# Performance work log

Hardware: AMD Instinct MI355X
Metric: run time of the kernel (lower is better)

The kernel has to match this reference:

```python
import jax, jax.numpy as jnp
import numpy as np

B, H, K, V = 64, 32, 128, 128


def setup_inputs() -> dict:
    key = jax.random.key(0)
    ks = jax.random.split(key, 7)
    q = jax.random.normal(ks[0], (B, 1, H, K), dtype=jnp.float32)
    k = jax.random.normal(ks[1], (B, 1, H, K), dtype=jnp.float32)
    v = jax.random.normal(ks[2], (B, 1, H, V), dtype=jnp.float32)
    # a = -kappa, b = kappa*a_gate in RWKV-7; plain gaussians suffice for a math reference
    a = jax.random.normal(ks[3], (B, 1, H, K), dtype=jnp.float32)
    b = jax.random.normal(ks[4], (B, 1, H, K), dtype=jnp.float32)
    # gk is a log-decay: negative so exp(gk) in (0, 1]
    gk = -jnp.abs(jax.random.normal(ks[5], (B, 1, H, K), dtype=jnp.float32)) * 0.1
    h0 = jax.random.normal(ks[6], (B, H, K, V), dtype=jnp.float32) * 0.1
    return {"q": q, "k": k, "v": v, "a": a, "b": b, "gk": gk, "h0": h0}


def reference(q, k, v, a, b, gk, h0):
    """RWKV-7 DPLR single-step (T=1) decode recurrence, per (batch, head):
      g     = exp(gk)                                # [K] decay
      s     = a^T H0                                 # [V]
      t     = (q*g)^T H0                             # [V]
      alpha = q . b ; beta = q . k                   # scalars
      o     = t + alpha*s + beta*v                   # [V]
      Ht    = diag(g) H0 + b s^T + k v^T             # [K,V]
    Mirrors dplr_decode_t1_kernel_streamK exactly (fp32 accumulation).
    """
    qf = q[:, 0].astype(jnp.float32)   # [B,H,K]
    kf = k[:, 0].astype(jnp.float32)
    af = a[:, 0].astype(jnp.float32)
    bf = b[:, 0].astype(jnp.float32)
    vf = v[:, 0].astype(jnp.float32)   # [B,H,V]
    g = jnp.exp(gk[:, 0].astype(jnp.float32))  # [B,H,K]
    hf = h0.astype(jnp.float32)        # [B,H,K,V]

    s = jnp.einsum('bhk,bhkv->bhv', af, hf)
    t = jnp.einsum('bhk,bhkv->bhv', qf * g, hf)
    alpha = jnp.sum(qf * bf, axis=-1, keepdims=True)  # [B,H,1]
    beta = jnp.sum(qf * kf, axis=-1, keepdims=True)   # [B,H,1]
    o = t + alpha * s + beta * vf                      # [B,H,V]

    ht = g[..., None] * hf + bf[..., None] * s[:, :, None, :] + kf[..., None] * vf[:, :, None, :]
    return o[:, None].astype(v.dtype), ht.astype(h0.dtype)
```

## Files before the change

kernel.cpp:

```cpp
#include <hip/hip_runtime.h>


#define KD 128
#define VD 128
#define BH_TOTAL 2048

__global__ __launch_bounds__(256, 4) void dplr_decode_t1_kernel(
    const float* __restrict__ q_,  const float* __restrict__ k_,
    const float* __restrict__ v_,  const float* __restrict__ a_,
    const float* __restrict__ b_,  const float* __restrict__ gk_,
    const float* __restrict__ h0_, float* __restrict__ out_)
{
    const int bh   = blockIdx.x >> 1;
    const int cb   = (blockIdx.x & 1) * 64;
    const int tid  = threadIdx.x;
    const int c    = (tid & 15) * 4;
    const int col  = cb + c;
    const int grp  = tid >> 4;
    const int r0   = grp * 8;
    const int wv   = tid >> 6;

    const size_t vec_off = (size_t)bh * KD;
    const size_t h_off   = (size_t)bh * (KD * VD);

    __shared__ float qs[KD], ks_[KD], bs[KD], as_[KD], gs[KD], qgs[KD];
    __shared__ float sred[4][64];
    __shared__ float tred[4][64];
    __shared__ float scomb[64];
    __shared__ float red2[2];

    float4 Hreg[8];
    const float* hp = h0_ + h_off + (size_t)r0 * VD + col;
#pragma unroll
    for (int j = 0; j < 8; ++j)
        Hreg[j] = *(const float4*)(hp + (size_t)j * VD);
    const float4 v4 = *(const float4*)(v_ + vec_off + col);

    if (tid < KD) {
        float qq = q_[vec_off + tid];
        float gg = __expf(gk_[vec_off + tid]);
        qs[tid]  = qq;
        ks_[tid] = k_[vec_off + tid];
        bs[tid]  = b_[vec_off + tid];
        as_[tid] = a_[vec_off + tid];
        gs[tid]  = gg;
        qgs[tid] = qq * gg;
    }
    __syncthreads();

    if (tid < 64) {
        float p = qs[tid] * bs[tid] + qs[tid + 64] * bs[tid + 64];
#pragma unroll
        for (int o = 32; o > 0; o >>= 1) p += __shfl_down(p, o, 64);
        if (tid == 0) red2[0] = p;
    } else if (tid < 128) {
        int l = tid - 64;
        float p = qs[l] * ks_[l] + qs[l + 64] * ks_[l + 64];
#pragma unroll
        for (int o = 32; o > 0; o >>= 1) p += __shfl_down(p, o, 64);
        if (l == 0) red2[1] = p;
    }

    float4 sp = make_float4(0.f, 0.f, 0.f, 0.f);
    float4 tp = make_float4(0.f, 0.f, 0.f, 0.f);
#pragma unroll
    for (int j = 0; j < 8; ++j) {
        const float av = as_[r0 + j];
        const float qg = qgs[r0 + j];
        const float4 h = Hreg[j];
        sp.x += av * h.x; sp.y += av * h.y; sp.z += av * h.z; sp.w += av * h.w;
        tp.x += qg * h.x; tp.y += qg * h.y; tp.z += qg * h.z; tp.w += qg * h.w;
    }

#pragma unroll
    for (int o = 16; o <= 32; o <<= 1) {
        sp.x += __shfl_xor(sp.x, o, 64); sp.y += __shfl_xor(sp.y, o, 64);
        sp.z += __shfl_xor(sp.z, o, 64); sp.w += __shfl_xor(sp.w, o, 64);
        tp.x += __shfl_xor(tp.x, o, 64); tp.y += __shfl_xor(tp.y, o, 64);
        tp.z += __shfl_xor(tp.z, o, 64); tp.w += __shfl_xor(tp.w, o, 64);
    }
    if ((tid & 63) < 16) {
        *(float4*)&sred[wv][c] = sp;
        *(float4*)&tred[wv][c] = tp;
    }
    __syncthreads();

    if (tid < 64) {
        float sc = sred[0][tid] + sred[1][tid] + sred[2][tid] + sred[3][tid];
        float tc = tred[0][tid] + tred[1][tid] + tred[2][tid] + tred[3][tid];
        scomb[tid] = sc;
        const float vv = v_[vec_off + cb + tid];
        out_[(size_t)bh * VD + cb + tid] = tc + red2[0] * sc + red2[1] * vv;
    }
    __syncthreads();

    const float4 s4 = *(const float4*)&scomb[c];
    float* op = out_ + (size_t)BH_TOTAL * VD + h_off + (size_t)r0 * VD + col;
#pragma unroll
    for (int j = 0; j < 8; ++j) {
        const int r = r0 + j;
        const float gr = gs[r];
        const float br = bs[r];
        const float kr = ks_[r];
        const float4 h = Hreg[j];
        float4 o4;
        o4.x = gr * h.x + br * s4.x + kr * v4.x;
        o4.y = gr * h.y + br * s4.y + kr * v4.y;
        o4.z = gr * h.z + br * s4.z + kr * v4.z;
        o4.w = gr * h.w + br * s4.w + kr * v4.w;
        *(float4*)(op + (size_t)j * VD) = o4;
    }
}

extern "C" void kernel_launch(void* const* d_in, const int* in_sizes, int n_in,
                              void* d_out, int out_size, void* d_ws, size_t ws_size,
                              hipStream_t stream) {
    const float* q  = (const float*)d_in[0];
    const float* k  = (const float*)d_in[1];
    const float* v  = (const float*)d_in[2];
    const float* a  = (const float*)d_in[3];
    const float* b  = (const float*)d_in[4];
    const float* gk = (const float*)d_in[5];
    const float* h0 = (const float*)d_in[6];
    float* out = (float*)d_out;

    dplr_decode_t1_kernel<<<BH_TOTAL * 2, 256, 0, stream>>>(q, k, v, a, b, gk, h0, out);
}
```

Before: 250.6 us.

## Make each wavefront own a 16-column slice and drop shared memory and barriers

```diff
diff --git a/kernel.cpp b/kernel.cpp
--- a/kernel.cpp
+++ b/kernel.cpp
@@ -11,104 +11,90 @@
     const float* __restrict__ b_,  const float* __restrict__ gk_,
     const float* __restrict__ h0_, float* __restrict__ out_)
 {
-    const int bh   = blockIdx.x >> 1;
-    const int cb   = (blockIdx.x & 1) * 64;
-    const int tid  = threadIdx.x;
-    const int c    = (tid & 15) * 4;
-    const int col  = cb + c;
-    const int grp  = tid >> 4;
-    const int r0   = grp * 8;
-    const int wv   = tid >> 6;
+    const int lane  = threadIdx.x & 63;
+    const int wid   = threadIdx.x >> 6;
+    const int gw    = blockIdx.x * 4 + wid;
+    const int bh    = gw >> 3;
+    const int slice = gw & 7;
+    const int cl    = lane & 3;
+    const int rg    = lane >> 2;
+    const int r0    = rg * 8;
+    const int col   = slice * 16 + cl * 4;
 
     const size_t vec_off = (size_t)bh * KD;
     const size_t h_off   = (size_t)bh * (KD * VD);
 
-    __shared__ float qs[KD], ks_[KD], bs[KD], as_[KD], gs[KD], qgs[KD];
-    __shared__ float sred[4][64];
-    __shared__ float tred[4][64];
-    __shared__ float scomb[64];
-    __shared__ float red2[2];
-
-    float4 Hreg[8];
     const float* hp = h0_ + h_off + (size_t)r0 * VD + col;
+    float4 H0r[8];
 #pragma unroll
     for (int j = 0; j < 8; ++j)
-        Hreg[j] = *(const float4*)(hp + (size_t)j * VD);
-    const float4 v4 = *(const float4*)(v_ + vec_off + col);
+        H0r[j] = *(const float4*)(hp + (size_t)j * VD);
 
-    if (tid < KD) {
-        float qq = q_[vec_off + tid];
-        float gg = __expf(gk_[vec_off + tid]);
-        qs[tid]  = qq;
-        ks_[tid] = k_[vec_off + tid];
-        bs[tid]  = b_[vec_off + tid];
-        as_[tid] = a_[vec_off + tid];
-        gs[tid]  = gg;
-        qgs[tid] = qq * gg;
-    }
-    __syncthreads();
+    const float4 v4  = *(const float4*)(v_  + vec_off + col);
+    const float4 qA  = *(const float4*)(q_  + vec_off + r0);
+    const float4 qB  = *(const float4*)(q_  + vec_off + r0 + 4);
+    const float4 gA  = *(const float4*)(gk_ + vec_off + r0);
+    const float4 gB  = *(const float4*)(gk_ + vec_off + r0 + 4);
+    const float4 aA  = *(const float4*)(a_  + vec_off + r0);
+    const float4 aB  = *(const float4*)(a_  + vec_off + r0 + 4);
+    const float4 kA  = *(const float4*)(k_  + vec_off + r0);
+    const float4 kB  = *(const float4*)(k_  + vec_off + r0 + 4);
+    const float4 bA  = *(const float4*)(b_  + vec_off + r0);
+    const float4 bB  = *(const float4*)(b_  + vec_off + r0 + 4);
 
-    if (tid < 64) {
-        float p = qs[tid] * bs[tid] + qs[tid + 64] * bs[tid + 64];
+    const float qv[8] = {qA.x, qA.y, qA.z, qA.w, qB.x, qB.y, qB.z, qB.w};
+    const float gkv[8]= {gA.x, gA.y, gA.z, gA.w, gB.x, gB.y, gB.z, gB.w};
+    const float av[8] = {aA.x, aA.y, aA.z, aA.w, aB.x, aB.y, aB.z, aB.w};
+    const float kv[8] = {kA.x, kA.y, kA.z, kA.w, kB.x, kB.y, kB.z, kB.w};
+    const float bv[8] = {bA.x, bA.y, bA.z, bA.w, bB.x, bB.y, bB.z, bB.w};
+
+    float g[8], qg[8];
 #pragma unroll
-        for (int o = 32; o > 0; o >>= 1) p += __shfl_down(p, o, 64);
-        if (tid == 0) red2[0] = p;
-    } else if (tid < 128) {
-        int l = tid - 64;
-        float p = qs[l] * ks_[l] + qs[l + 64] * ks_[l + 64];
-#pragma unroll
-        for (int o = 32; o > 0; o >>= 1) p += __shfl_down(p, o, 64);
-        if (l == 0) red2[1] = p;
-    }
+    for (int j = 0; j < 8; ++j) { g[j] = __expf(gkv[j]); qg[j] = qv[j] * g[j]; }
 
     float4 sp = make_float4(0.f, 0.f, 0.f, 0.f);
     float4 tp = make_float4(0.f, 0.f, 0.f, 0.f);
+    float pab = 0.f, pqk = 0.f;
 #pragma unroll
     for (int j = 0; j < 8; ++j) {
-        const float av = as_[r0 + j];
-        const float qg = qgs[r0 + j];
-        const float4 h = Hreg[j];
-        sp.x += av * h.x; sp.y += av * h.y; sp.z += av * h.z; sp.w += av * h.w;
-        tp.x += qg * h.x; tp.y += qg * h.y; tp.z += qg * h.z; tp.w += qg * h.w;
+        const float4 h = H0r[j];
+        sp.x += av[j] * h.x; sp.y += av[j] * h.y;
+        sp.z += av[j] * h.z; sp.w += av[j] * h.w;
+        tp.x += qg[j] * h.x; tp.y += qg[j] * h.y;
+        tp.z += qg[j] * h.z; tp.w += qg[j] * h.w;
+        pab  += qv[j] * bv[j];
+        pqk  += qv[j] * kv[j];
     }
 
 #pragma unroll
-    for (int o = 16; o <= 32; o <<= 1) {
-        sp.x += __shfl_xor(sp.x, o, 64); sp.y += __shfl_xor(sp.y, o, 64);
-        sp.z += __shfl_xor(sp.z, o, 64); sp.w += __shfl_xor(sp.w, o, 64);
-        tp.x += __shfl_xor(tp.x, o, 64); tp.y += __shfl_xor(tp.y, o, 64);
-        tp.z += __shfl_xor(tp.z, o, 64); tp.w += __shfl_xor(tp.w, o, 64);
+    for (int m = 4; m <= 32; m <<= 1) {
+        sp.x += __shfl_xor(sp.x, m, 64); sp.y += __shfl_xor(sp.y, m, 64);
+        sp.z += __shfl_xor(sp.z, m, 64); sp.w += __shfl_xor(sp.w, m, 64);
+        tp.x += __shfl_xor(tp.x, m, 64); tp.y += __shfl_xor(tp.y, m, 64);
+        tp.z += __shfl_xor(tp.z, m, 64); tp.w += __shfl_xor(tp.w, m, 64);
+        pab  += __shfl_xor(pab,  m, 64);
+        pqk  += __shfl_xor(pqk,  m, 64);
     }
-    if ((tid & 63) < 16) {
-        *(float4*)&sred[wv][c] = sp;
-        *(float4*)&tred[wv][c] = tp;
+
+    if (rg == 0) {
+        float4 o4;
+        o4.x = tp.x + pab * sp.x + pqk * v4.x;
+        o4.y = tp.y + pab * sp.y + pqk * v4.y;
+        o4.z = tp.z + pab * sp.z + pqk * v4.z;
+        o4.w = tp.w + pab * sp.w + pqk * v4.w;
+        *(float4*)(out_ + (size_t)bh * VD + col) = o4;
     }
-    __syncthreads();
 
-    if (tid < 64) {
-        float sc = sred[0][tid] + sred[1][tid] + sred[2][tid] + sred[3][tid];
-        float tc = tred[0][tid] + tred[1][tid] + tred[2][tid] + tred[3][tid];
-        scomb[tid] = sc;
-        const float vv = v_[vec_off + cb + tid];
-        out_[(size_t)bh * VD + cb + tid] = tc + red2[0] * sc + red2[1] * vv;
-    }
-    __syncthreads();
-
-    const float4 s4 = *(const float4*)&scomb[c];
     float* op = out_ + (size_t)BH_TOTAL * VD + h_off + (size_t)r0 * VD + col;
 #pragma unroll
     for (int j = 0; j < 8; ++j) {
-        const int r = r0 + j;
-        const float gr = gs[r];
-        const float br = bs[r];
-        const float kr = ks_[r];
-        const float4 h = Hreg[j];
-        float4 o4;
-        o4.x = gr * h.x + br * s4.x + kr * v4.x;
-        o4.y = gr * h.y + br * s4.y + kr * v4.y;
-        o4.z = gr * h.z + br * s4.z + kr * v4.z;
-        o4.w = gr * h.w + br * s4.w + kr * v4.w;
-        *(float4*)(op + (size_t)j * VD) = o4;
+        const float4 h = H0r[j];
+        float4 w;
+        w.x = g[j] * h.x + bv[j] * sp.x + kv[j] * v4.x;
+        w.y = g[j] * h.y + bv[j] * sp.y + kv[j] * v4.y;
+        w.z = g[j] * h.z + bv[j] * sp.z + kv[j] * v4.z;
+        w.w = g[j] * h.w + bv[j] * sp.w + kv[j] * v4.w;
+        *(float4*)(op + (size_t)j * VD) = w;
     }
 }
 
@@ -124,5 +110,5 @@
     const float* h0 = (const float*)d_in[6];
     float* out = (float*)d_out;
 
-    dplr_decode_t1_kernel<<<BH_TOTAL * 2, 256, 0, stream>>>(q, k, v, a, b, gk, h0, out);
+    dplr_decode_t1_kernel<<<BH_TOTAL * 8 / 4, 256, 0, stream>>>(q, k, v, a, b, gk, h0, out);
 }
```

Measured after the change: 253.5 us. About the same (+1.2%).
